# Kernel tuning notes

Measured on AMD Instinct MI355X. Metric: run time of the kernel, lower is better.

## Reference

```python
import jax, jax.numpy as jnp
import numpy as np

B, Cin, Cout, T, H, W = 8, 64, 64, 16, 32, 32
AH = 64  # attention_hidden_dims


def setup_inputs() -> dict:
    key = jax.random.key(0)
    ks = jax.random.split(key, 6)
    s = 0.05
    return {
        "X": jax.random.normal(ks[0], (B, Cin, T, H, W), jnp.float32),
        # 1x1 conv weights of the SelfAttention module (bias zero-init like nn.Conv2d default is uniform, but zeros is fine for a reference baseline)
        "q_w": jax.random.normal(ks[1], (AH, Cin), jnp.float32) * s,
        "q_b": jnp.zeros((AH,), jnp.float32),
        "k_w": jax.random.normal(ks[2], (AH, Cin), jnp.float32) * s,
        "k_b": jnp.zeros((AH,), jnp.float32),
        "v_w": jax.random.normal(ks[3], (Cin, Cin), jnp.float32) * s,
        "v_b": jnp.zeros((Cin,), jnp.float32),
        # ConvLSTM gate conv: concat([x, h]) -> 4*Cout channels, 3x3, padding 1
        "conv_w": jax.random.normal(ks[4], (4 * Cout, Cin + Cout, 3, 3), jnp.float32) * s,
        "conv_b": jnp.zeros((4 * Cout,), jnp.float32),
        # peephole weights, zero-init per WeightsInitializer.Zeros
        "w_ci": jnp.zeros((Cout, H, W), jnp.float32),
        "w_cf": jnp.zeros((Cout, H, W), jnp.float32),
        "w_co": jnp.zeros((Cout, H, W), jnp.float32),
    }


def _self_attention(x, q_w, q_b, k_w, k_b, v_w, v_b):
    # x: (B, Cin, H, W). 1x1 convs expressed as channel contractions.
    b, c, h, w = x.shape
    xf = x.reshape(b, c, h * w)                                    # (B, C, HW)
    q = jnp.einsum('oc,bcn->bno', q_w, xf) + q_b                   # (B, HW, AH)
    k = jnp.einsum('oc,bcn->bon', k_w, xf) + k_b[None, :, None]    # (B, AH, HW)
    v = jnp.einsum('oc,bcn->bon', v_w, xf) + v_b[None, :, None]    # (B, Cin, HW)
    attn = jax.nn.softmax(jnp.einsum('bno,bom->bnm', q, k), axis=-1)  # (B, HW, HW)
    out = jnp.einsum('bnm,bcm->bcn', attn, v).reshape(b, c, h, w)  # (B, Cin, H, W)
    return out, attn


def _convlstm_cell(x, h, c, conv_w, conv_b, w_ci, w_cf, w_co):
    z = jnp.concatenate([x, h], axis=1)  # (B, Cin+Cout, H, W)
    conv = jax.lax.conv_general_dilated(
        z, conv_w, window_strides=(1, 1), padding='SAME',
        dimension_numbers=('NCHW', 'OIHW', 'NCHW')) + conv_b[None, :, None, None]
    i_c, f_c, g_c, o_c = jnp.split(conv, 4, axis=1)
    i = jax.nn.sigmoid(i_c + w_ci * c)
    f = jax.nn.sigmoid(f_c + w_cf * c)
    new_c = f * c + i * jnp.tanh(g_c)
    o = jax.nn.sigmoid(o_c + w_co * new_c)
    new_h = o * jnp.tanh(new_c)
    return new_h, new_c


def reference(X, q_w, q_b, k_w, k_b, v_w, v_b, conv_w, conv_b, w_ci, w_cf, w_co):
    b = X.shape[0]
    h0 = jnp.zeros((b, Cout, H, W), X.dtype)
    c0 = jnp.zeros_like(h0)
    xs = jnp.moveaxis(X, 2, 0)  # (T, B, Cin, H, W) for scan over time

    def step(carry, x_t):
        h, c = carry
        ax, _ = _self_attention(x_t, q_w, q_b, k_w, k_b, v_w, v_b)
        new_h, new_c = _convlstm_cell(ax, h, c, conv_w, conv_b, w_ci, w_cf, w_co)
        return (new_h, new_c), new_h

    _, hs = jax.lax.scan(step, (h0, c0), xs)  # hs: (T, B, Cout, H, W)
    return jnp.moveaxis(hs, 0, 2)  # (B, Cout, T, H, W)
```

## Files before the change

kernel.cpp:

```cpp
#include <hip/hip_runtime.h>
#include <math.h>

typedef __attribute__((ext_vector_type(8))) __bf16 bf16x8;
typedef __attribute__((ext_vector_type(4))) float f32x4;
typedef unsigned short u16;
typedef unsigned int u32;

#define MFMA16(a, b, c) __builtin_amdgcn_mfma_f32_16x16x32_bf16(a, b, c, 0, 0, 0)

__device__ __forceinline__ u16 f2bf(float f) {
    u32 u = __float_as_uint(f);
    return (u16)((u + 0x7fffu + ((u >> 16) & 1u)) >> 16);
}
__device__ __forceinline__ float bf2f(u16 h) {
    return __uint_as_float(((u32)h) << 16);
}

__device__ __forceinline__ void gload16(const void* g, void* lds) {
    __builtin_amdgcn_global_load_lds(
        (const __attribute__((address_space(1))) unsigned int*)g,
        (__attribute__((address_space(3))) unsigned int*)lds, 16, 0, 0);
}

__global__ __launch_bounds__(256) void k_wtrans2(const float* __restrict__ cw,
                                                 u16* __restrict__ whi,
                                                 u16* __restrict__ wlo) {
    int idx = blockIdx.x * 256 + threadIdx.x;
    if (idx >= 294912) return;
    int s   = idx >> 15;
    int ocp = (idx >> 7) & 255;
    int ic  = idx & 127;
    int q = ocp >> 5, cc = (ocp >> 2) & 7, g = ocp & 3;
    int oc = g * 64 + q * 8 + cc;
    float f = cw[oc * 1152 + ic * 9 + s];
    u16 hi = f2bf(f);
    whi[idx] = hi;
    wlo[idx] = f2bf(f - bf2f(hi));
}

__global__ __launch_bounds__(256) void k_qkvw(
    const float* __restrict__ qw, const float* __restrict__ kw,
    const float* __restrict__ vw, u16* __restrict__ w2h, u16* __restrict__ w2l)
{
    int idx = blockIdx.x * 256 + threadIdx.x;
    if (idx >= 12288) return;
    int o = idx >> 6, c = idx & 63;
    float f = (o < 64) ? qw[o * 64 + c]
            : (o < 128) ? kw[(o - 64) * 64 + c]
                        : vw[(o - 128) * 64 + c];
    u16 hi = f2bf(f);
    w2h[idx] = hi;
    w2l[idx] = f2bf(f - bf2f(hi));
}

__global__ __launch_bounds__(256) void k_qkv2(
    const float* __restrict__ X,
    const u16* __restrict__ w2h, const u16* __restrict__ w2l,
    const float* __restrict__ qb, const float* __restrict__ kb,
    const float* __restrict__ vb,
    u16* __restrict__ qmat, u16* __restrict__ kmat, u16* __restrict__ vt)
{
    __shared__ u16 bhs[4096];
    __shared__ u16 bls[4096];

    const int tid = threadIdx.x;
    const int ns = blockIdx.x;
    const int bt = blockIdx.y;
    const int b = bt >> 4, t = bt & 15;
    const int n0 = ns * 64;

    const float* xb = X + (size_t)b * 1048576 + (size_t)t * 1024 + n0;
    for (int i = tid; i < 4096; i += 256) {
        int c = i >> 6, n = i & 63;
        float f = xb[(size_t)c * 16384 + n];
        u16 hi = f2bf(f);
        u16 lo = f2bf(f - bf2f(hi));
        int ci = c ^ ((n & 7) << 3);
        bhs[n * 64 + ci] = hi;
        bls[n * 64 + ci] = lo;
    }
    __syncthreads();

    const int wv = tid >> 6, lane = tid & 63;
    const int l15 = lane & 15, l4 = lane >> 4;
    const int o0 = wv * 48;

    f32x4 acc[3][4];
#pragma unroll
    for (int ot = 0; ot < 3; ++ot)
#pragma unroll
        for (int nt = 0; nt < 4; ++nt) acc[ot][nt] = (f32x4){0.f, 0.f, 0.f, 0.f};

#pragma unroll
    for (int kk = 0; kk < 2; ++kk) {
        bf16x8 Ah[3], Al[3];
#pragma unroll
        for (int ot = 0; ot < 3; ++ot) {
            int off = (o0 + ot * 16 + l15) * 64 + kk * 32 + l4 * 8;
            Ah[ot] = *reinterpret_cast<const bf16x8*>(w2h + off);
            Al[ot] = *reinterpret_cast<const bf16x8*>(w2l + off);
        }
#pragma unroll
        for (int nt = 0; nt < 4; ++nt) {
            int n = nt * 16 + l15;
            int gran = (kk * 4 + l4) ^ (n & 7);
            bf16x8 Bh = *reinterpret_cast<const bf16x8*>(bhs + n * 64 + gran * 8);
            bf16x8 Bl = *reinterpret_cast<const bf16x8*>(bls + n * 64 + gran * 8);
#pragma unroll
            for (int ot = 0; ot < 3; ++ot) {
                acc[ot][nt] = MFMA16(Ah[ot], Bh, acc[ot][nt]);
                acc[ot][nt] = MFMA16(Ah[ot], Bl, acc[ot][nt]);
                acc[ot][nt] = MFMA16(Al[ot], Bh, acc[ot][nt]);
            }
        }
    }

#pragma unroll
    for (int ot = 0; ot < 3; ++ot) {
#pragma unroll
        for (int r = 0; r < 4; ++r) {
            int row = o0 + ot * 16 + l4 * 4 + r;
            float bias = (row < 64) ? qb[row]
                       : (row < 128) ? kb[row - 64] : vb[row - 128];
#pragma unroll
            for (int nt = 0; nt < 4; ++nt) {
                int col = n0 + nt * 16 + l15;
                u16 h = f2bf(acc[ot][nt][r] + bias);
                if (row < 64)
                    qmat[(size_t)bt * 65536 + (size_t)col * 64 + row] = h;
                else if (row < 128)
                    kmat[(size_t)bt * 65536 + (size_t)col * 64 + (row - 64)] = h;
                else
                    vt[(size_t)bt * 65536 + (size_t)(row - 128) * 1024 + col] = h;
            }
        }
    }
}

__global__ __launch_bounds__(512, 2) void k_attn2(
    const u16* __restrict__ qmat, const u16* __restrict__ kmat,
    const u16* __restrict__ vt, u16* __restrict__ za)
{
    __shared__ char kl[16384];
    __shared__ char vl[16384];
    __shared__ u16 plds[8 * 16 * 40];

    const int tid = threadIdx.x;
    const int id  = blockIdx.x;
    const int w   = (id & 7) * 128 + (id >> 3);
    const int bt  = w >> 3;
    const int nt8 = w & 7;

    const int wv = tid >> 6, lane = tid & 63;
    const int l15 = lane & 15, l4 = lane >> 4;
    const int n0 = nt8 * 128 + wv * 16;

    const u16* qb_ = qmat + (size_t)bt * 65536;
    const u16* kb_ = kmat + (size_t)bt * 65536;
    const u16* vb_ = vt + (size_t)bt * 65536;
    u16* zab = za + (size_t)bt * 147968;

    if (nt8 == 0) {
        for (int j = tid; j < 2112; j += 512) {
            int pi = j >> 4, q16 = j & 15;
            int px = (pi < 34) ? pi
                   : (pi < 68) ? (33 * 34 + (pi - 34))
                               : ((1 + ((pi - 68) >> 1)) * 34 + ((pi - 68) & 1) * 33);
            *reinterpret_cast<uint4*>(zab + px * 128 + q16 * 8) =
                make_uint4(0u, 0u, 0u, 0u);
        }
    }

    bf16x8 qf0 = *reinterpret_cast<const bf16x8*>(qb_ + (n0 + l15) * 64 + l4 * 8);
    bf16x8 qf1 = *reinterpret_cast<const bf16x8*>(qb_ + (n0 + l15) * 64 + 32 + l4 * 8);

    f32x4 oacc[4];
#pragma unroll
    for (int ct = 0; ct < 4; ++ct) oacc[ct] = (f32x4){0.f, 0.f, 0.f, 0.f};
    float lsum = 0.f;
    char* plc = (char*)plds + wv * 1280;

    bf16x8 kst[2], vst[2];
#pragma unroll
    for (int r = 0; r < 2; ++r) {
        int c = tid + r * 512;
        kst[r] = *reinterpret_cast<const bf16x8*>(kb_ + (c >> 3) * 64 + (c & 7) * 8);
        vst[r] = *reinterpret_cast<const bf16x8*>(vb_ + (c >> 4) * 1024 + (c & 15) * 8);
    }

    for (int mt = 0; mt < 8; ++mt) {
        __syncthreads();
#pragma unroll
        for (int r = 0; r < 2; ++r) {
            int c = tid + r * 512;
            int m = c >> 3, sl = c & 7;
            *reinterpret_cast<bf16x8*>(kl + ((m * 128 + sl * 16) ^ ((m & 7) << 4))) = kst[r];
            int cc = c >> 4, sl2 = c & 15;
            *reinterpret_cast<bf16x8*>(vl + ((cc * 256 + sl2 * 16) ^ ((cc & 7) << 4))) = vst[r];
        }
        __syncthreads();
        if (mt < 7) {
            int mg = (mt + 1) * 128;
#pragma unroll
            for (int r = 0; r < 2; ++r) {
                int c = tid + r * 512;
                kst[r] = *reinterpret_cast<const bf16x8*>(kb_ + (mg + (c >> 3)) * 64 + (c & 7) * 8);
                vst[r] = *reinterpret_cast<const bf16x8*>(vb_ + (c >> 4) * 1024 + mg + (c & 15) * 8);
            }
        }

#pragma unroll
        for (int mi2 = 0; mi2 < 4; ++mi2) {
#pragma unroll
            for (int hf = 0; hf < 2; ++hf) {
                int ml = (mi2 * 2 + hf) * 16 + l15;
                f32x4 s = {0.f, 0.f, 0.f, 0.f};
                bf16x8 ka0 = *reinterpret_cast<const bf16x8*>(
                    kl + ((ml * 128 + l4 * 16) ^ ((ml & 7) << 4)));
                bf16x8 ka1 = *reinterpret_cast<const bf16x8*>(
                    kl + ((ml * 128 + 64 + l4 * 16) ^ ((ml & 7) << 4)));
                s = MFMA16(ka0, qf0, s);
                s = MFMA16(ka1, qf1, s);
                float p0 = __expf(s[0]);
                float p1 = __expf(s[1]);
                float p2 = __expf(s[2]);
                float p3 = __expf(s[3]);
                lsum += (p0 + p1) + (p2 + p3);
                u32 pa = (u32)f2bf(p0) | ((u32)f2bf(p1) << 16);
                u32 pb = (u32)f2bf(p2) | ((u32)f2bf(p3) << 16);
                *reinterpret_cast<uint2*>(plc + l15 * 80 + hf * 32 + l4 * 8) =
                    make_uint2(pa, pb);
            }
            bf16x8 pfrag = *reinterpret_cast<const bf16x8*>(plc + l15 * 80 + l4 * 16);
#pragma unroll
            for (int ct = 0; ct < 4; ++ct) {
                bf16x8 vfrag = *reinterpret_cast<const bf16x8*>(
                    vl + (((ct * 16 + l15) * 256 + mi2 * 64 + l4 * 16) ^ ((l15 & 7) << 4)));
                oacc[ct] = MFMA16(pfrag, vfrag, oacc[ct]);
            }
        }
    }

    lsum += __shfl_xor(lsum, 16, 64);
    lsum += __shfl_xor(lsum, 32, 64);

#pragma unroll
    for (int r = 0; r < 4; ++r) {
        float linv = 1.f / __shfl(lsum, l4 * 4 + r, 64);
        int nrow = n0 + l4 * 4 + r;
        u16* base = zab + (((nrow >> 5) + 1) * 34 + (nrow & 31) + 1) * 128;
#pragma unroll
        for (int ct = 0; ct < 4; ++ct) {
            float v = oacc[ct][r] * linv;
            u16 hi = f2bf(v);
            base[ct * 16 + l15]      = hi;
            base[64 + ct * 16 + l15] = f2bf(v - bf2f(hi));
        }
    }
}

__global__ __launch_bounds__(256) void k_cell7(
    const u16* __restrict__ za, const u16* __restrict__ zh_in,
    u16* __restrict__ zh_out, float* __restrict__ cst,
    const u16* __restrict__ whi, const u16* __restrict__ wlo,
    const float* __restrict__ conv_b,
    const float* __restrict__ wci, const float* __restrict__ wcf,
    const float* __restrict__ wco, float* __restrict__ out, int t)
{
    __shared__ __align__(16) char zt[104448];

    const int tid = threadIdx.x;
    const int id  = blockIdx.x;
    const int w   = (id & 7) * 32 + (id >> 3);
    const int b   = w >> 5;
    const int oq  = (w >> 3) & 3;
    const int ys  = w & 7;
    const int y0  = ys * 4;
    const int bt  = b * 16 + t;

    const int wv = tid >> 6, lane = tid & 63;
    const int l15 = lane & 15, l4 = lane >> 4;

    const u16* zab = za + (size_t)bt * 147968;
    const u16* zhb = zh_in + (size_t)b * 147968;

    for (int i = wv; i < 102; i += 4) {
        int j = i * 64 + lane;
        int p = j >> 5, sl = j & 31;
        int sls = (sl & 24) | ((sl ^ (p & 7)) & 7);
        int ly = p / 34, col = p - ly * 34;
        int gp = (y0 + ly) * 34 + col;
        int span = (sls >> 4) & 1;
        int ic8 = sls & 15;
        const u16* src = ((ic8 < 8) ? zab : zhb) + gp * 128 + span * 64 + (ic8 & 7) * 8;
        gload16(src, zt + i * 1024);
    }
    __syncthreads();

    f32x4 acc[4][2];
#pragma unroll
    for (int at = 0; at < 4; ++at)
#pragma unroll
        for (int nt = 0; nt < 2; ++nt) acc[at][nt] = (f32x4){0.f, 0.f, 0.f, 0.f};

    bf16x8 Ah[2][4], Al[2][4], Bh[2][2], Bl[2][2];

    auto loadA = [&](int set, int s, int ck) {
#pragma unroll
        for (int at = 0; at < 4; ++at) {
            size_t woff = (size_t)(s * 256 + oq * 64 + at * 16 + l15) * 128
                          + ck * 32 + l4 * 8;
            Ah[set][at] = *reinterpret_cast<const bf16x8*>(whi + woff);
            Al[set][at] = *reinterpret_cast<const bf16x8*>(wlo + woff);
        }
    };
    auto loadB = [&](int set, int s, int ck) {
        const int dy = s / 3 - 1, dx = s % 3 - 1;
        const int gs = ck * 4 + l4;
#pragma unroll
        for (int nt = 0; nt < 2; ++nt) {
            int pxl = (wv + dy + 1) * 34 + nt * 16 + l15 + 1 + dx;
            int sl = (gs & 8) | ((gs ^ (pxl & 7)) & 7);
            const char* bp = zt + pxl * 512 + sl * 16;
            Bh[set][nt] = *reinterpret_cast<const bf16x8*>(bp);
            Bl[set][nt] = *reinterpret_cast<const bf16x8*>(bp + 256);
        }
    };

    loadA(0, 0, 0);
    loadB(0, 0, 0);
#pragma unroll
    for (int ck = 0; ck < 4; ++ck) {
#pragma unroll
        for (int s = 0; s < 9; ++s) {
            const int cur = (ck + s) & 1, nxt = cur ^ 1;
            if (s < 8)      { loadA(nxt, s + 1, ck); loadB(nxt, s + 1, ck); }
            else if (ck < 3){ loadA(nxt, 0, ck + 1); loadB(nxt, 0, ck + 1); }
#pragma unroll
            for (int at = 0; at < 4; ++at)
#pragma unroll
                for (int nt = 0; nt < 2; ++nt) {
                    acc[at][nt] = MFMA16(Ah[cur][at], Bh[cur][nt], acc[at][nt]);
                    acc[at][nt] = MFMA16(Ah[cur][at], Bl[cur][nt], acc[at][nt]);
                    acc[at][nt] = MFMA16(Al[cur][at], Bh[cur][nt], acc[at][nt]);
                }
        }
    }

    u16* zho = zh_out + (size_t)b * 147968;
    const int y = y0 + wv;
#pragma unroll
    for (int at = 0; at < 4; ++at) {
        int ch = (oq * 2 + (at >> 1)) * 8 + (at & 1) * 4 + l4;
        float bi = conv_b[ch], bf = conv_b[64 + ch];
        float bg = conv_b[128 + ch], bo = conv_b[192 + ch];
#pragma unroll
        for (int nt = 0; nt < 2; ++nt) {
            int x = nt * 16 + l15;
            int n = y * 32 + x;
            float ci = acc[at][nt][0] + bi;
            float cf = acc[at][nt][1] + bf;
            float cg = acc[at][nt][2] + bg;
            float co = acc[at][nt][3] + bo;
            size_t si = ((size_t)b * 64 + ch) * 1024 + n;
            int pw_ = ch * 1024 + n;
            float cp = cst[si];
            float iv = 1.f / (1.f + __expf(-(ci + wci[pw_] * cp)));
            float fv = 1.f / (1.f + __expf(-(cf + wcf[pw_] * cp)));
            float nc = fv * cp + iv * tanhf(cg);
            float ov = 1.f / (1.f + __expf(-(co + wco[pw_] * nc)));
            float nh = ov * tanhf(nc);
            cst[si] = nc;
            out[(((size_t)b * 64 + ch) * 16 + t) * 1024 + n] = nh;
            u16 hhi = f2bf(nh);
            u16* zp = zho + ((y + 1) * 34 + (x + 1)) * 128;
            zp[ch]      = hhi;
            zp[64 + ch] = f2bf(nh - bf2f(hhi));
        }
    }
}

#define OB_Q    0ull
#define OB_K    16777216ull
#define OB_V    33554432ull
#define OB_ZA   50331648ull
#define OB_ZH0  88211456ull
#define OB_ZH1  90578944ull
#define OB_CST  92946432ull
#define OB_WHI  95043584ull
#define OB_WLO  95633408ull
#define OB_WQ2H 96223232ull
#define OB_WQ2L 96247808ull

extern "C" void kernel_launch(void* const* d_in, const int* in_sizes, int n_in,
                              void* d_out, int out_size, void* d_ws, size_t ws_size,
                              hipStream_t stream)
{
    const float* X   = (const float*)d_in[0];
    const float* qw  = (const float*)d_in[1];
    const float* qb  = (const float*)d_in[2];
    const float* kw  = (const float*)d_in[3];
    const float* kb  = (const float*)d_in[4];
    const float* vw  = (const float*)d_in[5];
    const float* vb  = (const float*)d_in[6];
    const float* cw  = (const float*)d_in[7];
    const float* cb  = (const float*)d_in[8];
    const float* wci = (const float*)d_in[9];
    const float* wcf = (const float*)d_in[10];
    const float* wco = (const float*)d_in[11];
    float* out = (float*)d_out;
    char* wsb  = (char*)d_ws;

    u16* qmat = (u16*)(wsb + OB_Q);
    u16* kmat = (u16*)(wsb + OB_K);
    u16* vt   = (u16*)(wsb + OB_V);
    u16* za   = (u16*)(wsb + OB_ZA);
    u16* zh0  = (u16*)(wsb + OB_ZH0);
    u16* zh1  = (u16*)(wsb + OB_ZH1);
    float* cst= (float*)(wsb + OB_CST);
    u16* whi  = (u16*)(wsb + OB_WHI);
    u16* wlo  = (u16*)(wsb + OB_WLO);
    u16* w2h  = (u16*)(wsb + OB_WQ2H);
    u16* w2l  = (u16*)(wsb + OB_WQ2L);

    hipMemsetAsync(zh0, 0, 6832128ull, stream);
    k_wtrans2<<<1152, 256, 0, stream>>>(cw, whi, wlo);
    k_qkvw<<<48, 256, 0, stream>>>(qw, kw, vw, w2h, w2l);
    k_qkv2<<<dim3(16, 128), 256, 0, stream>>>(X, w2h, w2l, qb, kb, vb,
                                              qmat, kmat, vt);
    k_attn2<<<1024, 512, 0, stream>>>(qmat, kmat, vt, za);

    for (int t = 0; t < 16; ++t) {
        u16* hin  = (t & 1) ? zh1 : zh0;
        u16* hout = (t & 1) ? zh0 : zh1;
        k_cell7<<<256, 256, 0, stream>>>(za, hin, hout, cst, whi, wlo,
                                         cb, wci, wcf, wco, out, t);
    }
}
```

Baseline: 722.6 us.

## Fuse ConvLSTM timesteps into cooperative kernel and double-buffer attention loads

The 16 per-timestep cell launches become one cooperative kernel that loops over time, keeps the cell state in registers and uses a grid-wide sync between steps. The aim is to remove launch overhead and the round trips of the cell state through global memory. The attention kernel now double-buffers K/V tiles in LDS with direct global-to-LDS loads, replacing the register staging and the extra barrier per tile. It also packs bf16 with a hardware convert instruction. In exchange it adds grid-sync cost and uses twice the LDS in attention, which could lower occupancy, and it falls back to per-step launches if the cooperative launch fails.

```diff
diff --git a/kernel.cpp b/kernel.cpp
--- a/kernel.cpp
+++ b/kernel.cpp
@@ -1,5 +1,8 @@
 #include <hip/hip_runtime.h>
+#include <hip/hip_cooperative_groups.h>
 #include <math.h>
+
+namespace cg = cooperative_groups;
 
 typedef __attribute__((ext_vector_type(8))) __bf16 bf16x8;
 typedef __attribute__((ext_vector_type(4))) float f32x4;
@@ -137,12 +140,14 @@
     }
 }
 
-__global__ __launch_bounds__(512, 2) void k_attn2(
+__global__ __launch_bounds__(512, 2) void k_attn3(
     const u16* __restrict__ qmat, const u16* __restrict__ kmat,
     const u16* __restrict__ vt, u16* __restrict__ za)
 {
-    __shared__ char kl[16384];
-    __shared__ char vl[16384];
+    __shared__ __align__(16) char kl0[16384];
+    __shared__ __align__(16) char kl1[16384];
+    __shared__ __align__(16) char vl0[16384];
+    __shared__ __align__(16) char vl1[16384];
     __shared__ u16 plds[8 * 16 * 40];
 
     const int tid = threadIdx.x;
@@ -174,40 +179,48 @@
     bf16x8 qf0 = *reinterpret_cast<const bf16x8*>(qb_ + (n0 + l15) * 64 + l4 * 8);
     bf16x8 qf1 = *reinterpret_cast<const bf16x8*>(qb_ + (n0 + l15) * 64 + 32 + l4 * 8);
 
+    auto issueK = [&](int mt_, char* dst) {
+#pragma unroll
+        for (int j = 0; j < 2; ++j) {
+            int s = wv * 128 + j * 64 + lane;
+            int m = s >> 3;
+            int d4 = (s & 7) ^ (m & 7);
+            gload16(kb_ + (mt_ * 128 + m) * 64 + d4 * 8,
+                    dst + (wv * 128 + j * 64) * 16);
+        }
+    };
+    auto issueV = [&](int mt_, char* dst) {
+#pragma unroll
+        for (int j = 0; j < 2; ++j) {
+            int s = wv * 128 + j * 64 + lane;
+            int c = s >> 4;
+            int m8 = (s & 8) | ((s ^ (c & 7)) & 7);
+            gload16(vb_ + c * 1024 + mt_ * 128 + m8 * 8,
+                    dst + (wv * 128 + j * 64) * 16);
+        }
+    };
+
     f32x4 oacc[4];
 #pragma unroll
     for (int ct = 0; ct < 4; ++ct) oacc[ct] = (f32x4){0.f, 0.f, 0.f, 0.f};
     float lsum = 0.f;
     char* plc = (char*)plds + wv * 1280;
 
-    bf16x8 kst[2], vst[2];
-#pragma unroll
-    for (int r = 0; r < 2; ++r) {
-        int c = tid + r * 512;
-        kst[r] = *reinterpret_cast<const bf16x8*>(kb_ + (c >> 3) * 64 + (c & 7) * 8);
-        vst[r] = *reinterpret_cast<const bf16x8*>(vb_ + (c >> 4) * 1024 + (c & 15) * 8);
-    }
+    issueK(0, kl0);
+    issueV(0, vl0);
 
     for (int mt = 0; mt < 8; ++mt) {
-        __syncthreads();
-#pragma unroll
-        for (int r = 0; r < 2; ++r) {
-            int c = tid + r * 512;
-            int m = c >> 3, sl = c & 7;
-            *reinterpret_cast<bf16x8*>(kl + ((m * 128 + sl * 16) ^ ((m & 7) << 4))) = kst[r];
-            int cc = c >> 4, sl2 = c & 15;
-            *reinterpret_cast<bf16x8*>(vl + ((cc * 256 + sl2 * 16) ^ ((cc & 7) << 4))) = vst[r];
-        }
-        __syncthreads();
+        char* klc = (mt & 1) ? kl1 : kl0;
+        char* vlc = (mt & 1) ? vl1 : vl0;
         if (mt < 7) {
-            int mg = (mt + 1) * 128;
-#pragma unroll
-            for (int r = 0; r < 2; ++r) {
-                int c = tid + r * 512;
-                kst[r] = *reinterpret_cast<const bf16x8*>(kb_ + (mg + (c >> 3)) * 64 + (c & 7) * 8);
-                vst[r] = *reinterpret_cast<const bf16x8*>(vb_ + (c >> 4) * 1024 + mg + (c & 15) * 8);
-            }
-        }
+            issueK(mt + 1, (mt & 1) ? kl0 : kl1);
+            issueV(mt + 1, (mt & 1) ? vl0 : vl1);
+            asm volatile("s_waitcnt vmcnt(4)" ::: "memory");
+        } else {
+            asm volatile("s_waitcnt vmcnt(0)" ::: "memory");
+        }
+        __builtin_amdgcn_s_barrier();
+        __builtin_amdgcn_sched_barrier(0);
 
 #pragma unroll
         for (int mi2 = 0; mi2 < 4; ++mi2) {
@@ -216,9 +229,9 @@
                 int ml = (mi2 * 2 + hf) * 16 + l15;
                 f32x4 s = {0.f, 0.f, 0.f, 0.f};
                 bf16x8 ka0 = *reinterpret_cast<const bf16x8*>(
-                    kl + ((ml * 128 + l4 * 16) ^ ((ml & 7) << 4)));
+                    klc + ((ml * 128 + l4 * 16) ^ ((ml & 7) << 4)));
                 bf16x8 ka1 = *reinterpret_cast<const bf16x8*>(
-                    kl + ((ml * 128 + 64 + l4 * 16) ^ ((ml & 7) << 4)));
+                    klc + ((ml * 128 + 64 + l4 * 16) ^ ((ml & 7) << 4)));
                 s = MFMA16(ka0, qf0, s);
                 s = MFMA16(ka1, qf1, s);
                 float p0 = __expf(s[0]);
@@ -226,8 +239,9 @@
                 float p2 = __expf(s[2]);
                 float p3 = __expf(s[3]);
                 lsum += (p0 + p1) + (p2 + p3);
-                u32 pa = (u32)f2bf(p0) | ((u32)f2bf(p1) << 16);
-                u32 pb = (u32)f2bf(p2) | ((u32)f2bf(p3) << 16);
+                u32 pa, pb;
+                asm("v_cvt_pk_bf16_f32 %0, %1, %2" : "=v"(pa) : "v"(p0), "v"(p1));
+                asm("v_cvt_pk_bf16_f32 %0, %1, %2" : "=v"(pb) : "v"(p2), "v"(p3));
                 *reinterpret_cast<uint2*>(plc + l15 * 80 + hf * 32 + l4 * 8) =
                     make_uint2(pa, pb);
             }
@@ -235,10 +249,11 @@
 #pragma unroll
             for (int ct = 0; ct < 4; ++ct) {
                 bf16x8 vfrag = *reinterpret_cast<const bf16x8*>(
-                    vl + (((ct * 16 + l15) * 256 + mi2 * 64 + l4 * 16) ^ ((l15 & 7) << 4)));
+                    vlc + (((ct * 16 + l15) * 256 + mi2 * 64 + l4 * 16) ^ ((l15 & 7) << 4)));
                 oacc[ct] = MFMA16(pfrag, vfrag, oacc[ct]);
             }
         }
+        __builtin_amdgcn_s_barrier();
     }
 
     lsum += __shfl_xor(lsum, 16, 64);
@@ -259,30 +274,14 @@
     }
 }
 
-__global__ __launch_bounds__(256) void k_cell7(
-    const u16* __restrict__ za, const u16* __restrict__ zh_in,
-    u16* __restrict__ zh_out, float* __restrict__ cst,
-    const u16* __restrict__ whi, const u16* __restrict__ wlo,
-    const float* __restrict__ conv_b,
-    const float* __restrict__ wci, const float* __restrict__ wcf,
-    const float* __restrict__ wco, float* __restrict__ out, int t)
-{
-    __shared__ __align__(16) char zt[104448];
-
-    const int tid = threadIdx.x;
-    const int id  = blockIdx.x;
-    const int w   = (id & 7) * 32 + (id >> 3);
-    const int b   = w >> 5;
-    const int oq  = (w >> 3) & 3;
-    const int ys  = w & 7;
-    const int y0  = ys * 4;
-    const int bt  = b * 16 + t;
-
-    const int wv = tid >> 6, lane = tid & 63;
+__device__ __forceinline__ void cell_body(
+    const u16* zab, const u16* zhb, u16* zho, char* zt,
+    const u16* whi, const u16* wlo, const float* conv_b,
+    const float* wci, const float* wcf, const float* wco,
+    float* out, int t, int b, int oq, int y0, int wv, int lane,
+    float* creg)
+{
     const int l15 = lane & 15, l4 = lane >> 4;
-
-    const u16* zab = za + (size_t)bt * 147968;
-    const u16* zhb = zh_in + (size_t)b * 147968;
 
     for (int i = wv; i < 102; i += 4) {
         int j = i * 64 + lane;
@@ -347,7 +346,6 @@
         }
     }
 
-    u16* zho = zh_out + (size_t)b * 147968;
     const int y = y0 + wv;
 #pragma unroll
     for (int at = 0; at < 4; ++at) {
@@ -362,15 +360,14 @@
             float cf = acc[at][nt][1] + bf;
             float cg = acc[at][nt][2] + bg;
             float co = acc[at][nt][3] + bo;
-            size_t si = ((size_t)b * 64 + ch) * 1024 + n;
             int pw_ = ch * 1024 + n;
-            float cp = cst[si];
+            float cp = creg[at * 2 + nt];
             float iv = 1.f / (1.f + __expf(-(ci + wci[pw_] * cp)));
             float fv = 1.f / (1.f + __expf(-(cf + wcf[pw_] * cp)));
             float nc = fv * cp + iv * tanhf(cg);
             float ov = 1.f / (1.f + __expf(-(co + wco[pw_] * nc)));
             float nh = ov * tanhf(nc);
-            cst[si] = nc;
+            creg[at * 2 + nt] = nc;
             out[(((size_t)b * 64 + ch) * 16 + t) * 1024 + n] = nh;
             u16 hhi = f2bf(nh);
             u16* zp = zho + ((y + 1) * 34 + (x + 1)) * 128;
@@ -378,6 +375,88 @@
             zp[64 + ch] = f2bf(nh - bf2f(hhi));
         }
     }
+}
+
+__global__ __launch_bounds__(256) void k_cell_coop(
+    const u16* __restrict__ za, u16* __restrict__ zh0, u16* __restrict__ zh1,
+    const u16* __restrict__ whi, const u16* __restrict__ wlo,
+    const float* __restrict__ conv_b,
+    const float* __restrict__ wci, const float* __restrict__ wcf,
+    const float* __restrict__ wco, float* __restrict__ out)
+{
+    __shared__ __align__(16) char zt[104448];
+
+    const int tid = threadIdx.x;
+    const int id  = blockIdx.x;
+    const int w   = (id & 7) * 32 + (id >> 3);
+    const int b   = w >> 5;
+    const int oq  = (w >> 3) & 3;
+    const int y0  = (w & 7) * 4;
+
+    const int wv = tid >> 6, lane = tid & 63;
+
+    float creg[8];
+#pragma unroll
+    for (int k = 0; k < 8; ++k) creg[k] = 0.f;
+
+    cg::grid_group grid = cg::this_grid();
+
+    for (int t = 0; t < 16; ++t) {
+        const u16* zab = za + (size_t)(b * 16 + t) * 147968;
+        const u16* zhb = ((t & 1) ? zh1 : zh0) + (size_t)b * 147968;
+        u16* zho       = ((t & 1) ? zh0 : zh1) + (size_t)b * 147968;
+        cell_body(zab, zhb, zho, zt, whi, wlo, conv_b, wci, wcf, wco,
+                  out, t, b, oq, y0, wv, lane, creg);
+        if (t < 15) {
+            __threadfence();
+            grid.sync();
+        }
+    }
+}
+
+__global__ __launch_bounds__(256) void k_cell7(
+    const u16* __restrict__ za, const u16* __restrict__ zh_in,
+    u16* __restrict__ zh_out, float* __restrict__ cst,
+    const u16* __restrict__ whi, const u16* __restrict__ wlo,
+    const float* __restrict__ conv_b,
+    const float* __restrict__ wci, const float* __restrict__ wcf,
+    const float* __restrict__ wco, float* __restrict__ out, int t)
+{
+    __shared__ __align__(16) char zt[104448];
+
+    const int tid = threadIdx.x;
+    const int id  = blockIdx.x;
+    const int w   = (id & 7) * 32 + (id >> 3);
+    const int b   = w >> 5;
+    const int oq  = (w >> 3) & 3;
+    const int y0  = (w & 7) * 4;
+    const int bt  = b * 16 + t;
+
+    const int wv = tid >> 6, lane = tid & 63;
+    const int l15 = lane & 15, l4 = lane >> 4;
+
+    float creg[8];
+#pragma unroll
+    for (int at = 0; at < 4; ++at)
+#pragma unroll
+        for (int nt = 0; nt < 2; ++nt) {
+            int ch = (oq * 2 + (at >> 1)) * 8 + (at & 1) * 4 + l4;
+            int n = (y0 + wv) * 32 + nt * 16 + l15;
+            creg[at * 2 + nt] = cst[((size_t)b * 64 + ch) * 1024 + n];
+        }
+
+    cell_body(za + (size_t)bt * 147968, zh_in + (size_t)b * 147968,
+              zh_out + (size_t)b * 147968, zt, whi, wlo, conv_b,
+              wci, wcf, wco, out, t, b, oq, y0, wv, lane, creg);
+
+#pragma unroll
+    for (int at = 0; at < 4; ++at)
+#pragma unroll
+        for (int nt = 0; nt < 2; ++nt) {
+            int ch = (oq * 2 + (at >> 1)) * 8 + (at & 1) * 4 + l4;
+            int n = (y0 + wv) * 32 + nt * 16 + l15;
+            cst[((size_t)b * 64 + ch) * 1024 + n] = creg[at * 2 + nt];
+        }
 }
 
 #define OB_Q    0ull
@@ -428,12 +507,20 @@
     k_qkvw<<<48, 256, 0, stream>>>(qw, kw, vw, w2h, w2l);
     k_qkv2<<<dim3(16, 128), 256, 0, stream>>>(X, w2h, w2l, qb, kb, vb,
                                               qmat, kmat, vt);
-    k_attn2<<<1024, 512, 0, stream>>>(qmat, kmat, vt, za);
-
-    for (int t = 0; t < 16; ++t) {
-        u16* hin  = (t & 1) ? zh1 : zh0;
-        u16* hout = (t & 1) ? zh0 : zh1;
-        k_cell7<<<256, 256, 0, stream>>>(za, hin, hout, cst, whi, wlo,
-                                         cb, wci, wcf, wco, out, t);
-    }
-}
+    k_attn3<<<1024, 512, 0, stream>>>(qmat, kmat, vt, za);
+
+    void* cargs[] = {(void*)&za, (void*)&zh0, (void*)&zh1, (void*)&whi,
+                     (void*)&wlo, (void*)&cb, (void*)&wci, (void*)&wcf,
+                     (void*)&wco, (void*)&out};
+    hipError_t ce = hipLaunchCooperativeKernel((const void*)k_cell_coop,
+                                               dim3(256), dim3(256),
+                                               cargs, 0u, stream);
+    if (ce != hipSuccess) {
+        for (int t = 0; t < 16; ++t) {
+            u16* hin  = (t & 1) ? zh1 : zh0;
+            u16* hout = (t & 1) ? zh0 : zh1;
+            k_cell7<<<256, 256, 0, stream>>>(za, hin, hout, cst, whi, wlo,
+                                             cb, wci, wcf, wco, out, t);
+        }
+    }
+}
```

Result: slower. 2.005 ms (+177.4%).

## Double-buffer attention K/V via direct global-to-LDS loads; halve cell tile rows

Applied to the files above, without the earlier changes.

The attention kernel now streams K and V tiles straight from global memory into two LDS buffers with global_load_lds. Waits use explicit vmcnt counters and barriers in place of staging through registers with two syncthreads per tile. The goal is to overlap the next tile's fetch with the current tile's MFMAs. Separately, the ConvLSTM cell kernel now covers 2 rows per block instead of 4 and launches 512 blocks, using less LDS and fewer accumulators. This gives the sequential per-timestep kernel more parallelism, at the cost of more redundant halo and weight loading.

```diff
diff --git a/kernel.cpp b/kernel.cpp
--- a/kernel.cpp
+++ b/kernel.cpp
@@ -137,12 +137,14 @@
     }
 }
 
-__global__ __launch_bounds__(512, 2) void k_attn2(
+__global__ __launch_bounds__(512, 2) void k_attn3(
     const u16* __restrict__ qmat, const u16* __restrict__ kmat,
     const u16* __restrict__ vt, u16* __restrict__ za)
 {
-    __shared__ char kl[16384];
-    __shared__ char vl[16384];
+    __shared__ __align__(16) char kl0[16384];
+    __shared__ __align__(16) char kl1[16384];
+    __shared__ __align__(16) char vl0[16384];
+    __shared__ __align__(16) char vl1[16384];
     __shared__ u16 plds[8 * 16 * 40];
 
     const int tid = threadIdx.x;
@@ -174,40 +176,48 @@
     bf16x8 qf0 = *reinterpret_cast<const bf16x8*>(qb_ + (n0 + l15) * 64 + l4 * 8);
     bf16x8 qf1 = *reinterpret_cast<const bf16x8*>(qb_ + (n0 + l15) * 64 + 32 + l4 * 8);
 
+    auto issueK = [&](int mt_, char* dst) {
+#pragma unroll
+        for (int j = 0; j < 2; ++j) {
+            int s = wv * 128 + j * 64 + lane;
+            int m = s >> 3;
+            int d4 = (s & 7) ^ (m & 7);
+            gload16(kb_ + (mt_ * 128 + m) * 64 + d4 * 8,
+                    dst + (wv * 128 + j * 64) * 16);
+        }
+    };
+    auto issueV = [&](int mt_, char* dst) {
+#pragma unroll
+        for (int j = 0; j < 2; ++j) {
+            int s = wv * 128 + j * 64 + lane;
+            int c = s >> 4;
+            int m8 = (s & 8) | ((s ^ (c & 7)) & 7);
+            gload16(vb_ + c * 1024 + mt_ * 128 + m8 * 8,
+                    dst + (wv * 128 + j * 64) * 16);
+        }
+    };
+
     f32x4 oacc[4];
 #pragma unroll
     for (int ct = 0; ct < 4; ++ct) oacc[ct] = (f32x4){0.f, 0.f, 0.f, 0.f};
     float lsum = 0.f;
     char* plc = (char*)plds + wv * 1280;
 
-    bf16x8 kst[2], vst[2];
-#pragma unroll
-    for (int r = 0; r < 2; ++r) {
-        int c = tid + r * 512;
-        kst[r] = *reinterpret_cast<const bf16x8*>(kb_ + (c >> 3) * 64 + (c & 7) * 8);
-        vst[r] = *reinterpret_cast<const bf16x8*>(vb_ + (c >> 4) * 1024 + (c & 15) * 8);
-    }
+    issueK(0, kl0);
+    issueV(0, vl0);
 
     for (int mt = 0; mt < 8; ++mt) {
-        __syncthreads();
-#pragma unroll
-        for (int r = 0; r < 2; ++r) {
-            int c = tid + r * 512;
-            int m = c >> 3, sl = c & 7;
-            *reinterpret_cast<bf16x8*>(kl + ((m * 128 + sl * 16) ^ ((m & 7) << 4))) = kst[r];
-            int cc = c >> 4, sl2 = c & 15;
-            *reinterpret_cast<bf16x8*>(vl + ((cc * 256 + sl2 * 16) ^ ((cc & 7) << 4))) = vst[r];
-        }
-        __syncthreads();
+        char* klc = (mt & 1) ? kl1 : kl0;
+        char* vlc = (mt & 1) ? vl1 : vl0;
         if (mt < 7) {
-            int mg = (mt + 1) * 128;
-#pragma unroll
-            for (int r = 0; r < 2; ++r) {
-                int c = tid + r * 512;
-                kst[r] = *reinterpret_cast<const bf16x8*>(kb_ + (mg + (c >> 3)) * 64 + (c & 7) * 8);
-                vst[r] = *reinterpret_cast<const bf16x8*>(vb_ + (c >> 4) * 1024 + mg + (c & 15) * 8);
-            }
-        }
+            issueK(mt + 1, (mt & 1) ? kl0 : kl1);
+            issueV(mt + 1, (mt & 1) ? vl0 : vl1);
+            asm volatile("s_waitcnt vmcnt(4)" ::: "memory");
+        } else {
+            asm volatile("s_waitcnt vmcnt(0)" ::: "memory");
+        }
+        __builtin_amdgcn_s_barrier();
+        __builtin_amdgcn_sched_barrier(0);
 
 #pragma unroll
         for (int mi2 = 0; mi2 < 4; ++mi2) {
@@ -216,9 +226,9 @@
                 int ml = (mi2 * 2 + hf) * 16 + l15;
                 f32x4 s = {0.f, 0.f, 0.f, 0.f};
                 bf16x8 ka0 = *reinterpret_cast<const bf16x8*>(
-                    kl + ((ml * 128 + l4 * 16) ^ ((ml & 7) << 4)));
+                    klc + ((ml * 128 + l4 * 16) ^ ((ml & 7) << 4)));
                 bf16x8 ka1 = *reinterpret_cast<const bf16x8*>(
-                    kl + ((ml * 128 + 64 + l4 * 16) ^ ((ml & 7) << 4)));
+                    klc + ((ml * 128 + 64 + l4 * 16) ^ ((ml & 7) << 4)));
                 s = MFMA16(ka0, qf0, s);
                 s = MFMA16(ka1, qf1, s);
                 float p0 = __expf(s[0]);
@@ -235,10 +245,11 @@
 #pragma unroll
             for (int ct = 0; ct < 4; ++ct) {
                 bf16x8 vfrag = *reinterpret_cast<const bf16x8*>(
-                    vl + (((ct * 16 + l15) * 256 + mi2 * 64 + l4 * 16) ^ ((l15 & 7) << 4)));
+                    vlc + (((ct * 16 + l15) * 256 + mi2 * 64 + l4 * 16) ^ ((l15 & 7) << 4)));
                 oacc[ct] = MFMA16(pfrag, vfrag, oacc[ct]);
             }
         }
+        __builtin_amdgcn_s_barrier();
     }
 
     lsum += __shfl_xor(lsum, 16, 64);
@@ -259,7 +270,7 @@
     }
 }
 
-__global__ __launch_bounds__(256) void k_cell7(
+__global__ __launch_bounds__(256) void k_cell8(
     const u16* __restrict__ za, const u16* __restrict__ zh_in,
     u16* __restrict__ zh_out, float* __restrict__ cst,
     const u16* __restrict__ whi, const u16* __restrict__ wlo,
@@ -267,15 +278,15 @@
     const float* __restrict__ wci, const float* __restrict__ wcf,
     const float* __restrict__ wco, float* __restrict__ out, int t)
 {
-    __shared__ __align__(16) char zt[104448];
+    __shared__ __align__(16) char zt[69632];
 
     const int tid = threadIdx.x;
     const int id  = blockIdx.x;
-    const int w   = (id & 7) * 32 + (id >> 3);
-    const int b   = w >> 5;
-    const int oq  = (w >> 3) & 3;
-    const int ys  = w & 7;
-    const int y0  = ys * 4;
+    const int w   = (id & 7) * 64 + (id >> 3);
+    const int b   = w >> 6;
+    const int oq  = (w >> 4) & 3;
+    const int ys  = w & 15;
+    const int y0  = ys * 2;
     const int bt  = b * 16 + t;
 
     const int wv = tid >> 6, lane = tid & 63;
@@ -284,7 +295,7 @@
     const u16* zab = za + (size_t)bt * 147968;
     const u16* zhb = zh_in + (size_t)b * 147968;
 
-    for (int i = wv; i < 102; i += 4) {
+    for (int i = wv; i < 68; i += 4) {
         int j = i * 64 + lane;
         int p = j >> 5, sl = j & 31;
         int sls = (sl & 24) | ((sl ^ (p & 7)) & 7);
@@ -297,13 +308,11 @@
     }
     __syncthreads();
 
-    f32x4 acc[4][2];
-#pragma unroll
-    for (int at = 0; at < 4; ++at)
-#pragma unroll
-        for (int nt = 0; nt < 2; ++nt) acc[at][nt] = (f32x4){0.f, 0.f, 0.f, 0.f};
-
-    bf16x8 Ah[2][4], Al[2][4], Bh[2][2], Bl[2][2];
+    f32x4 acc[4];
+#pragma unroll
+    for (int at = 0; at < 4; ++at) acc[at] = (f32x4){0.f, 0.f, 0.f, 0.f};
+
+    bf16x8 Ah[2][4], Al[2][4], Bh[2], Bl[2];
 
     auto loadA = [&](int set, int s, int ck) {
 #pragma unroll
@@ -317,14 +326,11 @@
     auto loadB = [&](int set, int s, int ck) {
         const int dy = s / 3 - 1, dx = s % 3 - 1;
         const int gs = ck * 4 + l4;
-#pragma unroll
-        for (int nt = 0; nt < 2; ++nt) {
-            int pxl = (wv + dy + 1) * 34 + nt * 16 + l15 + 1 + dx;
-            int sl = (gs & 8) | ((gs ^ (pxl & 7)) & 7);
-            const char* bp = zt + pxl * 512 + sl * 16;
-            Bh[set][nt] = *reinterpret_cast<const bf16x8*>(bp);
-            Bl[set][nt] = *reinterpret_cast<const bf16x8*>(bp + 256);
-        }
+        int pxl = ((wv >> 1) + dy + 1) * 34 + (wv & 1) * 16 + l15 + 1 + dx;
+        int sl = (gs & 8) | ((gs ^ (pxl & 7)) & 7);
+        const char* bp = zt + pxl * 512 + sl * 16;
+        Bh[set] = *reinterpret_cast<const bf16x8*>(bp);
+        Bl[set] = *reinterpret_cast<const bf16x8*>(bp + 256);
     };
 
     loadA(0, 0, 0);
@@ -337,46 +343,39 @@
             if (s < 8)      { loadA(nxt, s + 1, ck); loadB(nxt, s + 1, ck); }
             else if (ck < 3){ loadA(nxt, 0, ck + 1); loadB(nxt, 0, ck + 1); }
 #pragma unroll
-            for (int at = 0; at < 4; ++at)
-#pragma unroll
-                for (int nt = 0; nt < 2; ++nt) {
-                    acc[at][nt] = MFMA16(Ah[cur][at], Bh[cur][nt], acc[at][nt]);
-                    acc[at][nt] = MFMA16(Ah[cur][at], Bl[cur][nt], acc[at][nt]);
-                    acc[at][nt] = MFMA16(Al[cur][at], Bh[cur][nt], acc[at][nt]);
-                }
+            for (int at = 0; at < 4; ++at) {
+                acc[at] = MFMA16(Ah[cur][at], Bh[cur], acc[at]);
+                acc[at] = MFMA16(Ah[cur][at], Bl[cur], acc[at]);
+                acc[at] = MFMA16(Al[cur][at], Bh[cur], acc[at]);
+            }
         }
     }
 
     u16* zho = zh_out + (size_t)b * 147968;
-    const int y = y0 + wv;
+    const int y = y0 + (wv >> 1);
+    const int x = (wv & 1) * 16 + l15;
+    const int n = y * 32 + x;
 #pragma unroll
     for (int at = 0; at < 4; ++at) {
         int ch = (oq * 2 + (at >> 1)) * 8 + (at & 1) * 4 + l4;
-        float bi = conv_b[ch], bf = conv_b[64 + ch];
-        float bg = conv_b[128 + ch], bo = conv_b[192 + ch];
-#pragma unroll
-        for (int nt = 0; nt < 2; ++nt) {
-            int x = nt * 16 + l15;
-            int n = y * 32 + x;
-            float ci = acc[at][nt][0] + bi;
-            float cf = acc[at][nt][1] + bf;
-            float cg = acc[at][nt][2] + bg;
-            float co = acc[at][nt][3] + bo;
-            size_t si = ((size_t)b * 64 + ch) * 1024 + n;
-            int pw_ = ch * 1024 + n;
-            float cp = cst[si];
-            float iv = 1.f / (1.f + __expf(-(ci + wci[pw_] * cp)));
-            float fv = 1.f / (1.f + __expf(-(cf + wcf[pw_] * cp)));
-            float nc = fv * cp + iv * tanhf(cg);
-            float ov = 1.f / (1.f + __expf(-(co + wco[pw_] * nc)));
-            float nh = ov * tanhf(nc);
-            cst[si] = nc;
-            out[(((size_t)b * 64 + ch) * 16 + t) * 1024 + n] = nh;
-            u16 hhi = f2bf(nh);
-            u16* zp = zho + ((y + 1) * 34 + (x + 1)) * 128;
-            zp[ch]      = hhi;
-            zp[64 + ch] = f2bf(nh - bf2f(hhi));
-        }
+        float ci = acc[at][0] + conv_b[ch];
+        float cf = acc[at][1] + conv_b[64 + ch];
+        float cg = acc[at][2] + conv_b[128 + ch];
+        float co = acc[at][3] + conv_b[192 + ch];
+        size_t si = ((size_t)b * 64 + ch) * 1024 + n;
+        int pw_ = ch * 1024 + n;
+        float cp = cst[si];
+        float iv = 1.f / (1.f + __expf(-(ci + wci[pw_] * cp)));
+        float fv = 1.f / (1.f + __expf(-(cf + wcf[pw_] * cp)));
+        float nc = fv * cp + iv * tanhf(cg);
+        float ov = 1.f / (1.f + __expf(-(co + wco[pw_] * nc)));
+        float nh = ov * tanhf(nc);
+        cst[si] = nc;
+        out[(((size_t)b * 64 + ch) * 16 + t) * 1024 + n] = nh;
+        u16 hhi = f2bf(nh);
+        u16* zp = zho + ((y + 1) * 34 + (x + 1)) * 128;
+        zp[ch]      = hhi;
+        zp[64 + ch] = f2bf(nh - bf2f(hhi));
     }
 }
 
@@ -428,12 +427,12 @@
     k_qkvw<<<48, 256, 0, stream>>>(qw, kw, vw, w2h, w2l);
     k_qkv2<<<dim3(16, 128), 256, 0, stream>>>(X, w2h, w2l, qb, kb, vb,
                                               qmat, kmat, vt);
-    k_attn2<<<1024, 512, 0, stream>>>(qmat, kmat, vt, za);
+    k_attn3<<<1024, 512, 0, stream>>>(qmat, kmat, vt, za);
 
     for (int t = 0; t < 16; ++t) {
         u16* hin  = (t & 1) ? zh1 : zh0;
         u16* hout = (t & 1) ? zh0 : zh1;
-        k_cell7<<<256, 256, 0, stream>>>(za, hin, hout, cst, whi, wlo,
+        k_cell8<<<512, 256, 0, stream>>>(za, hin, hout, cst, whi, wlo,
                                          cb, wci, wcf, wco, out, t);
     }
 }
```

After: 1.213 ms. +67.9%, slower.
